# Optimization experiments

Hardware: AMD Instinct MI355X
Metric: run time of the kernel (lower is better)

The kernel has to match this reference:

```python
import jax, jax.numpy as jnp
import numpy as np


def setup_inputs() -> dict:
    key = jax.random.key(0)
    ks = jax.random.split(key, 4)
    N, T, D, H = 64, 512, 1024, 1024
    x = jax.random.normal(ks[0], (N, T, D), dtype=jnp.float32)
    h0 = jax.random.normal(ks[1], (N, H), dtype=jnp.float32)
    Wx = jax.random.normal(ks[2], (D, 4 * H), dtype=jnp.float32) / np.sqrt(D)
    Wh = jax.random.normal(ks[3], (H, 4 * H), dtype=jnp.float32) / np.sqrt(H)
    b = jnp.zeros((4 * H,), dtype=jnp.float32)
    return {"x": x, "h0": h0, "Wx": Wx, "Wh": Wh, "b": b}


def reference(x, h0, Wx, Wh, b):
    # x: [N, T, D]; h0: [N, H]; Wx: [D, 4H]; Wh: [H, 4H]; b: [4H]
    H = h0.shape[1]
    # Batch the input-to-hidden matmul over all timesteps at once: [N, T, 4H]
    xW = jnp.einsum('ntd,df->ntf', x, Wx) + b
    c0 = jnp.zeros_like(h0)

    def step(carry, xw_t):
        prev_h, prev_c = carry
        preact = xw_t + prev_h @ Wh           # [N, 4H]
        ai, af, ao, ag = jnp.split(preact, 4, axis=1)
        i = jax.nn.sigmoid(ai)
        f = jax.nn.sigmoid(af)
        o = jax.nn.sigmoid(ao)
        g = jnp.tanh(ag)
        next_c = f * prev_c + i * g
        next_h = o * jnp.tanh(next_c)
        return (next_h, next_c), next_h

    # scan over time: move T to leading axis
    _, hs = jax.lax.scan(step, (h0, c0), jnp.swapaxes(xW, 0, 1))
    return jnp.swapaxes(hs, 0, 1)  # [N, T, H]
```

## Files before the change

kernel.cpp:

```cpp
#include <hip/hip_runtime.h>
#include <cstdint>
#include <cstddef>

#define N_ 64
#define T_ 512
#define D_ 1024
#define H_ 1024
#define FH 4096

typedef __attribute__((ext_vector_type(8))) short bf16x8;
typedef __attribute__((ext_vector_type(4))) float f32x4;

static __device__ __forceinline__ uint16_t f2bf_(float f) {
  union { float f; uint32_t u; } v; v.f = f;
  uint32_t u = v.u + 0x7FFFu + ((v.u >> 16) & 1u);
  return (uint16_t)(u >> 16);
}
static __device__ __forceinline__ float bf2f_(uint16_t s) {
  union { uint32_t u; float f; } v; v.u = ((uint32_t)s) << 16;
  return v.f;
}
static __device__ __forceinline__ void unpk2_(unsigned long long e,
                                              uint32_t& hi, uint32_t& lo) {
  uint32_t a = (uint32_t)e, b = (uint32_t)(e >> 32);
  hi = (a >> 16) | (b & 0xFFFF0000u);
  lo = (a & 0xFFFFu) | (b << 16);
}
static __device__ __forceinline__ void cvt8_(const float* p, bf16x8& hv,
                                             bf16x8& lv) {
  float4 v0 = *reinterpret_cast<const float4*>(p);
  float4 v1 = *reinterpret_cast<const float4*>(p + 4);
  float f[8] = {v0.x, v0.y, v0.z, v0.w, v1.x, v1.y, v1.z, v1.w};
#pragma unroll
  for (int e = 0; e < 8; ++e) {
    ushort h = f2bf_(f[e]);
    hv[e] = (short)h;
    lv[e] = (short)f2bf_(f[e] - bf2f_(h));
  }
}

#define ALD(p) (*(p))

__global__ __launch_bounds__(256) void pack_w_k(const float* __restrict__ W,
                                                ushort* __restrict__ hi,
                                                ushort* __restrict__ lo) {
  const int i = blockIdx.x * 256 + threadIdx.x;
  const int lane = i & 63, kc = (i >> 6) & 31, bid = i >> 11;
  const int c = lane & 15;
  const int col = (c >> 2) * H_ + (bid << 2) + (c & 3);
  const int k0 = (kc << 5) + ((lane >> 4) << 3);
  const size_t o = ((size_t)(bid * 32 + kc) * 64 + lane) * 8;
#pragma unroll
  for (int e = 0; e < 8; ++e) {
    float v = W[(size_t)(k0 + e) * FH + col];
    ushort h = f2bf_(v);
    hi[o + e] = h;
    lo[o + e] = f2bf_(v - bf2f_(h));
  }
}

__global__ __launch_bounds__(256) void conv_h0pk_k(const float* __restrict__ src,
                                                   uint32_t* __restrict__ dst,
                                                   unsigned* bar) {
  if (blockIdx.x == 0) {
    bar[threadIdx.x] = 0u;
    if (threadIdx.x < 8) bar[384 + 32 * threadIdx.x] = 0u;
  }
  const int i = blockIdx.x * 256 + threadIdx.x;
  float4 v = reinterpret_cast<const float4*>(src)[i];
  uint4 o;
  { ushort h = f2bf_(v.x); o.x = ((uint32_t)h << 16) | f2bf_(v.x - bf2f_(h)); }
  { ushort h = f2bf_(v.y); o.y = ((uint32_t)h << 16) | f2bf_(v.y - bf2f_(h)); }
  { ushort h = f2bf_(v.z); o.z = ((uint32_t)h << 16) | f2bf_(v.z - bf2f_(h)); }
  { ushort h = f2bf_(v.w); o.w = ((uint32_t)h << 16) | f2bf_(v.w - bf2f_(h)); }
  reinterpret_cast<uint4*>(dst)[i] = o;
}

__global__ __launch_bounds__(256) void gemm_xw_mfma(
    const ushort* __restrict__ Wxh, const ushort* __restrict__ Wxl,
    const float* __restrict__ x, const float* __restrict__ bias,
    uint32_t* __restrict__ xwp, int tb) {
  const int bid = blockIdx.x;
  const int tl = blockIdx.y << 2;
  const int t0 = tb + tl;
  const int tid = threadIdx.x, lane = tid & 63, mt = tid >> 6;
  const int row = (mt << 4) | (lane & 15);
  const int kg = lane >> 4;

  const bf16x8* Bh = reinterpret_cast<const bf16x8*>(Wxh) + (size_t)bid * 2048 + lane;
  const bf16x8* Bl = reinterpret_cast<const bf16x8*>(Wxl) + (size_t)bid * 2048 + lane;
  const float* ax = x + ((size_t)row * T_ + t0) * D_ + (kg << 3);

  f32x4 xa0 = {0.f, 0.f, 0.f, 0.f};
  f32x4 xa1 = {0.f, 0.f, 0.f, 0.f};
  f32x4 xa2 = {0.f, 0.f, 0.f, 0.f};
  f32x4 xa3 = {0.f, 0.f, 0.f, 0.f};
#pragma unroll 2
  for (int kc = 0; kc < 32; ++kc) {
    bf16x8 bh = Bh[kc << 6];
    bf16x8 bl = Bl[kc << 6];
    bf16x8 h0, l0, h1, l1, h2, l2, h3, l3;
    cvt8_(ax + (kc << 5), h0, l0);
    cvt8_(ax + D_ + (kc << 5), h1, l1);
    cvt8_(ax + 2 * D_ + (kc << 5), h2, l2);
    cvt8_(ax + 3 * D_ + (kc << 5), h3, l3);
    xa0 = __builtin_amdgcn_mfma_f32_16x16x32_bf16(h0, bh, xa0, 0, 0, 0);
    xa1 = __builtin_amdgcn_mfma_f32_16x16x32_bf16(h1, bh, xa1, 0, 0, 0);
    xa2 = __builtin_amdgcn_mfma_f32_16x16x32_bf16(h2, bh, xa2, 0, 0, 0);
    xa3 = __builtin_amdgcn_mfma_f32_16x16x32_bf16(h3, bh, xa3, 0, 0, 0);
    xa0 = __builtin_amdgcn_mfma_f32_16x16x32_bf16(h0, bl, xa0, 0, 0, 0);
    xa1 = __builtin_amdgcn_mfma_f32_16x16x32_bf16(h1, bl, xa1, 0, 0, 0);
    xa2 = __builtin_amdgcn_mfma_f32_16x16x32_bf16(h2, bl, xa2, 0, 0, 0);
    xa3 = __builtin_amdgcn_mfma_f32_16x16x32_bf16(h3, bl, xa3, 0, 0, 0);
    xa0 = __builtin_amdgcn_mfma_f32_16x16x32_bf16(l0, bh, xa0, 0, 0, 0);
    xa1 = __builtin_amdgcn_mfma_f32_16x16x32_bf16(l1, bh, xa1, 0, 0, 0);
    xa2 = __builtin_amdgcn_mfma_f32_16x16x32_bf16(l2, bh, xa2, 0, 0, 0);
    xa3 = __builtin_amdgcn_mfma_f32_16x16x32_bf16(l3, bh, xa3, 0, 0, 0);
  }

  const int dc = lane & 15, dr = (lane >> 4) << 2;
  const int g = dc >> 2, jj = dc & 3;
  const float bv = bias[g * H_ + (bid << 2) + jj];
#pragma unroll
  for (int r = 0; r < 4; ++r) {
    const int rw = (mt << 4) + dr + r;
    const size_t o = ((size_t)tl * 256 + bid) * 1024 + rw * 16 + jj * 4 + g;
    float v0 = xa0[r] + bv, v1 = xa1[r] + bv, v2 = xa2[r] + bv, v3 = xa3[r] + bv;
    ushort h;
    h = f2bf_(v0); xwp[o] = ((uint32_t)h << 16) | f2bf_(v0 - bf2f_(h));
    h = f2bf_(v1); xwp[o + 262144] = ((uint32_t)h << 16) | f2bf_(v1 - bf2f_(h));
    h = f2bf_(v2); xwp[o + 2 * 262144] = ((uint32_t)h << 16) | f2bf_(v2 - bf2f_(h));
    h = f2bf_(v3); xwp[o + 3 * 262144] = ((uint32_t)h << 16) | f2bf_(v3 - bf2f_(h));
  }
}

__global__ __launch_bounds__(512, 2) void lstm_scan_k(
    const ushort* __restrict__ Whh_g, const ushort* __restrict__ Whl_g,
    const uint32_t* __restrict__ xwp,
    uint32_t* __restrict__ hseq, float* __restrict__ cbuf,
    float* __restrict__ out, unsigned* __restrict__ bar, int tb) {
  extern __shared__ char ldsraw[];
  bf16x8* const WhH = (bf16x8*)ldsraw;
  bf16x8* const WhL = WhH + 2048;
  float* const pre = (float*)(WhL + 2048);

  const int tid = threadIdx.x, bid = blockIdx.x;
  const int lane = tid & 63, w = tid >> 6;
  const int mt = w & 3, kh = w >> 2;
  const int khb = kh << 4;
  const int arow = (mt << 4) | (lane & 15);
  const int kg = lane >> 4;
  const int dc = lane & 15, dr = (lane >> 4) << 2;
  const int en = tid >> 2, ejj = tid & 3;

  unsigned* const relmy = bar + 384 + ((bid & 7) << 5);

  {
    const bf16x8* gh = reinterpret_cast<const bf16x8*>(Whh_g) + (size_t)bid * 2048;
    const bf16x8* gl = reinterpret_cast<const bf16x8*>(Whl_g) + (size_t)bid * 2048;
#pragma unroll
    for (int r = 0; r < 4; ++r) {
      int u = tid + (r << 9);
      WhH[u] = gh[u];
      WhL[u] = gl[u];
    }
  }
  __syncthreads();

  for (int tl = 0; tl < 256; ++tl) {
    const int t = tb + tl;
    f32x4 acc0 = {0.f, 0.f, 0.f, 0.f};
    f32x4 acc1 = {0.f, 0.f, 0.f, 0.f};
    const unsigned long long* Apk =
        (const unsigned long long*)(hseq + (size_t)t * 65536) +
        arow * 512 + (kh << 8) + kg * 4;

    unsigned long long pa0, pa1, pa2, pa3, pb0, pb1, pb2, pb3;
    unsigned long long pc0, pc1, pc2, pc3, pd0, pd1, pd2, pd3;
    unsigned long long qa0, qa1, qa2, qa3, qb0, qb1, qb2, qb3;
    unsigned long long qc0, qc1, qc2, qc3, qd0, qd1, qd2, qd3;

#define HLD(P, CH)                                                            \
  {                                                                           \
    const unsigned long long* ap_ = Apk + ((CH) << 6);                        \
    P##a0 = ALD(ap_ + 0);  P##a1 = ALD(ap_ + 1);                              \
    P##a2 = ALD(ap_ + 2);  P##a3 = ALD(ap_ + 3);                              \
    P##b0 = ALD(ap_ + 16); P##b1 = ALD(ap_ + 17);                             \
    P##b2 = ALD(ap_ + 18); P##b3 = ALD(ap_ + 19);                             \
    P##c0 = ALD(ap_ + 32); P##c1 = ALD(ap_ + 33);                             \
    P##c2 = ALD(ap_ + 34); P##c3 = ALD(ap_ + 35);                             \
    P##d0 = ALD(ap_ + 48); P##d1 = ALD(ap_ + 49);                             \
    P##d2 = ALD(ap_ + 50); P##d3 = ALD(ap_ + 51);                             \
  }

#define HKC(E0, E1, E2, E3, KCG, ACC)                                         \
  {                                                                           \
    union { uint32_t u[4]; bf16x8 v; } fh_, fl_;                              \
    unpk2_(E0, fh_.u[0], fl_.u[0]);                                           \
    unpk2_(E1, fh_.u[1], fl_.u[1]);                                           \
    unpk2_(E2, fh_.u[2], fl_.u[2]);                                           \
    unpk2_(E3, fh_.u[3], fl_.u[3]);                                           \
    bf16x8 bh_ = WhH[((KCG) << 6) + lane];                                    \
    bf16x8 bl_ = WhL[((KCG) << 6) + lane];                                    \
    ACC = __builtin_amdgcn_mfma_f32_16x16x32_bf16(fh_.v, bh_, ACC, 0, 0, 0);  \
    ACC = __builtin_amdgcn_mfma_f32_16x16x32_bf16(fh_.v, bl_, ACC, 0, 0, 0);  \
    ACC = __builtin_amdgcn_mfma_f32_16x16x32_bf16(fl_.v, bh_, ACC, 0, 0, 0);  \
  }

#define HCOMP(P, CH)                                                          \
  HKC(P##a0, P##a1, P##a2, P##a3, khb + (CH) * 4 + 0, acc0)                   \
  HKC(P##b0, P##b1, P##b2, P##b3, khb + (CH) * 4 + 1, acc1)                   \
  HKC(P##c0, P##c1, P##c2, P##c3, khb + (CH) * 4 + 2, acc0)                   \
  HKC(P##d0, P##d1, P##d2, P##d3, khb + (CH) * 4 + 3, acc1)

    HLD(p, 0)
    HLD(q, 1) HCOMP(p, 0)
    HLD(p, 2) HCOMP(q, 1)
    HLD(q, 3) HCOMP(p, 2)
    HCOMP(q, 3)
#undef HLD
#undef HKC
#undef HCOMP

    f32x4 accs = acc0 + acc1;
#pragma unroll
    for (int r = 0; r < 4; ++r)
      pre[((kh << 6) + (mt << 4) + dr + r) * 17 + dc] = accs[r];
    __syncthreads();

    if (tid < 256) {
      const uint4 xp = *reinterpret_cast<const uint4*>(
          xwp + (size_t)tl * 262144 + (size_t)bid * 1024 + en * 16 + ejj * 4);
      float a0 = pre[en * 17 + ejj] + pre[(64 + en) * 17 + ejj] +
                 bf2f_((ushort)(xp.x >> 16)) + bf2f_((ushort)(xp.x & 0xFFFF));
      float a1 = pre[en * 17 + 4 + ejj] + pre[(64 + en) * 17 + 4 + ejj] +
                 bf2f_((ushort)(xp.y >> 16)) + bf2f_((ushort)(xp.y & 0xFFFF));
      float a2 = pre[en * 17 + 8 + ejj] + pre[(64 + en) * 17 + 8 + ejj] +
                 bf2f_((ushort)(xp.z >> 16)) + bf2f_((ushort)(xp.z & 0xFFFF));
      float a3 = pre[en * 17 + 12 + ejj] + pre[(64 + en) * 17 + 12 + ejj] +
                 bf2f_((ushort)(xp.w >> 16)) + bf2f_((ushort)(xp.w & 0xFFFF));
      const int hx = en * H_ + (bid << 2) + ejj;
      float cp = (t == 0) ? 0.f : cbuf[hx];
      float iv = 1.f / (1.f + __expf(-a0));
      float fv = 1.f / (1.f + __expf(-a1));
      float ov = 1.f / (1.f + __expf(-a2));
      float gv = tanhf(a3);
      float cn = fmaf(fv, cp, iv * gv);
      cbuf[hx] = cn;
      float hn = ov * tanhf(cn);
      out[(size_t)en * ((size_t)T_ * H_) + (size_t)t * H_ + (bid << 2) + ejj] = hn;
      ushort hh = f2bf_(hn);
      uint32_t pk = ((uint32_t)hh << 16) | f2bf_(hn - bf2f_(hh));
      __hip_atomic_store(&hseq[(size_t)(t + 1) * 65536 + hx], pk,
                         __ATOMIC_RELAXED, __HIP_MEMORY_SCOPE_AGENT);
    }

    asm volatile("s_waitcnt vmcnt(0)" ::: "memory");
    __syncthreads();

    const unsigned tgt = (unsigned)(t + 1);
    if (tid == 0)
      __hip_atomic_store(&bar[bid], tgt, __ATOMIC_RELAXED,
                         __HIP_MEMORY_SCOPE_AGENT);
    if (bid == 0 && tid < 64) {
      const unsigned long long* fl = (const unsigned long long*)bar;
      for (;;) {
        unsigned long long v0 = __hip_atomic_load(fl + tid, __ATOMIC_RELAXED,
                                                  __HIP_MEMORY_SCOPE_AGENT);
        unsigned long long v1 = __hip_atomic_load(fl + 64 + tid, __ATOMIC_RELAXED,
                                                  __HIP_MEMORY_SCOPE_AGENT);
        bool ok = ((unsigned)v0 >= tgt) && ((unsigned)(v0 >> 32) >= tgt) &&
                  ((unsigned)v1 >= tgt) && ((unsigned)(v1 >> 32) >= tgt);
        if (__all((int)ok)) break;
      }
      if (tid < 8)
        __hip_atomic_store(bar + 384 + (tid << 5), tgt, __ATOMIC_RELAXED,
                           __HIP_MEMORY_SCOPE_AGENT);
    }
    if (tid == 0) {
      while (__hip_atomic_load(relmy, __ATOMIC_RELAXED,
                               __HIP_MEMORY_SCOPE_AGENT) < tgt)
        __builtin_amdgcn_s_sleep(1);
    }
    __syncthreads();
  }
}

__global__ __launch_bounds__(256) void lstm_step_fb(
    const float* __restrict__ xt, const float* __restrict__ Wx,
    const float* __restrict__ Wh, const float* __restrict__ bias,
    const float* __restrict__ h_prev, long long hstride,
    float* __restrict__ cbuf, float* __restrict__ h_out, int first) {
  __shared__ float hS[32][128];
  __shared__ float wT[32][132];
  __shared__ float pre[32][34];
  const int tid = threadIdx.x;
  const int colblk = blockIdx.x & 127;
  const int nh = blockIdx.x >> 7;
  const int j0 = colblk << 3;
  const int n0 = nh << 5;
  const int ng = tid >> 4, cg2 = tid & 15;
  const int na = ng << 1, ca = cg2 << 1;

  float acc[2][2] = {{0.f, 0.f}, {0.f, 0.f}};

#pragma unroll
  for (int pr = 0; pr < 2; ++pr) {
    const float* src = (pr == 0) ? h_prev : xt;
    long long sstr = (pr == 0) ? hstride : (long long)T_ * D_;
    const float* W = (pr == 0) ? Wh : Wx;
    for (int k0 = 0; k0 < 1024; k0 += 128) {
      __syncthreads();
#pragma unroll
      for (int p = 0; p < 4; ++p) {
        int idx = tid + (p << 8);
        int r = idx >> 5, c4 = (idx & 31) << 2;
        *reinterpret_cast<float4*>(&hS[r][c4]) =
            *reinterpret_cast<const float4*>(src + (size_t)(n0 + r) * sstr + k0 + c4);
      }
#pragma unroll
      for (int p = 0; p < 4; ++p) {
        int idx = tid + (p << 8);
        int k = idx >> 3, sub = idx & 7;
        int g = sub >> 1, hf = (sub & 1) << 2;
        float4 v = *reinterpret_cast<const float4*>(
            W + (size_t)(k0 + k) * FH + g * H_ + j0 + hf);
        int cb = (g << 3) + hf;
        wT[cb][k] = v.x; wT[cb + 1][k] = v.y; wT[cb + 2][k] = v.z; wT[cb + 3][k] = v.w;
      }
      __syncthreads();
#pragma unroll
      for (int kk = 0; kk < 128; kk += 4) {
        float4 h0v = *reinterpret_cast<const float4*>(&hS[na][kk]);
        float4 h1v = *reinterpret_cast<const float4*>(&hS[na + 1][kk]);
        float4 w0 = *reinterpret_cast<const float4*>(&wT[ca][kk]);
        float4 w1 = *reinterpret_cast<const float4*>(&wT[ca + 1][kk]);
        acc[0][0] = fmaf(h0v.x, w0.x, acc[0][0]); acc[0][0] = fmaf(h0v.y, w0.y, acc[0][0]);
        acc[0][0] = fmaf(h0v.z, w0.z, acc[0][0]); acc[0][0] = fmaf(h0v.w, w0.w, acc[0][0]);
        acc[0][1] = fmaf(h0v.x, w1.x, acc[0][1]); acc[0][1] = fmaf(h0v.y, w1.y, acc[0][1]);
        acc[0][1] = fmaf(h0v.z, w1.z, acc[0][1]); acc[0][1] = fmaf(h0v.w, w1.w, acc[0][1]);
        acc[1][0] = fmaf(h1v.x, w0.x, acc[1][0]); acc[1][0] = fmaf(h1v.y, w0.y, acc[1][0]);
        acc[1][0] = fmaf(h1v.z, w0.z, acc[1][0]); acc[1][0] = fmaf(h1v.w, w0.w, acc[1][0]);
        acc[1][1] = fmaf(h1v.x, w1.x, acc[1][1]); acc[1][1] = fmaf(h1v.y, w1.y, acc[1][1]);
        acc[1][1] = fmaf(h1v.z, w1.z, acc[1][1]); acc[1][1] = fmaf(h1v.w, w1.w, acc[1][1]);
      }
    }
  }

  pre[na][ca] = acc[0][0];
  pre[na][ca + 1] = acc[0][1];
  pre[na + 1][ca] = acc[1][0];
  pre[na + 1][ca + 1] = acc[1][1];
  __syncthreads();

  const int nl = tid >> 3, jl = tid & 7;
  const int n = n0 + nl;
  const int jg = j0 + jl;
  float ai = pre[nl][jl] + bias[jg];
  float af = pre[nl][8 + jl] + bias[H_ + jg];
  float ao = pre[nl][16 + jl] + bias[2 * H_ + jg];
  float ag = pre[nl][24 + jl] + bias[3 * H_ + jg];
  float cp = first ? 0.0f : cbuf[n * H_ + jg];
  float iv = 1.f / (1.f + __expf(-ai));
  float fv = 1.f / (1.f + __expf(-af));
  float ov = 1.f / (1.f + __expf(-ao));
  float gv = tanhf(ag);
  float cn = fmaf(fv, cp, iv * gv);
  cbuf[n * H_ + jg] = cn;
  h_out[(size_t)n * ((size_t)T_ * H_) + jg] = ov * tanhf(cn);
}

extern "C" void kernel_launch(void* const* d_in, const int* in_sizes, int n_in,
                              void* d_out, int out_size, void* d_ws, size_t ws_size,
                              hipStream_t stream) {
  (void)in_sizes; (void)n_in; (void)out_size;
  const float* x  = (const float*)d_in[0];
  const float* h0 = (const float*)d_in[1];
  const float* Wx = (const float*)d_in[2];
  const float* Wh = (const float*)d_in[3];
  const float* b  = (const float*)d_in[4];
  float* out = (float*)d_out;

  const size_t MB = 1u << 20;
  char* p = (char*)d_ws;

  if (ws_size >= 420 * MB) {
    unsigned* bar = (unsigned*)p;
    ushort* Whh = (ushort*)(p + 1 * MB);
    ushort* Whl = (ushort*)(p + 9 * MB);
    ushort* Wxh = (ushort*)(p + 17 * MB);
    ushort* Wxl = (ushort*)(p + 25 * MB);
    uint32_t* hseq = (uint32_t*)(p + 33 * MB);
    float* cbuf = (float*)(p + 162 * MB);
    uint32_t* xwp = (uint32_t*)(p + 163 * MB);

    pack_w_k<<<dim3(2048), dim3(256), 0, stream>>>(Wh, Whh, Whl);
    pack_w_k<<<dim3(2048), dim3(256), 0, stream>>>(Wx, Wxh, Wxl);
    conv_h0pk_k<<<dim3(64), dim3(256), 0, stream>>>(h0, hseq, bar);

    const unsigned SH = 2048 * 16 * 2 + 128 * 17 * 4;
    hipFuncSetAttribute((const void*)lstm_scan_k,
                        hipFuncAttributeMaxDynamicSharedMemorySize, (int)SH);

    gemm_xw_mfma<<<dim3(256, 64), dim3(256), 0, stream>>>(Wxh, Wxl, x, b, xwp, 0);
    lstm_scan_k<<<dim3(256), dim3(512), SH, stream>>>(Whh, Whl, xwp, hseq, cbuf,
                                                      out, bar, 0);
    gemm_xw_mfma<<<dim3(256, 64), dim3(256), 0, stream>>>(Wxh, Wxl, x, b, xwp, 256);
    lstm_scan_k<<<dim3(256), dim3(512), SH, stream>>>(Whh, Whl, xwp, hseq, cbuf,
                                                      out, bar, 256);
  } else {
    float* cbuf = (float*)p;
    for (int t = 0; t < T_; ++t) {
      const float* hp = (t == 0) ? h0 : out + (size_t)(t - 1) * H_;
      long long hstr = (t == 0) ? (long long)H_ : (long long)T_ * H_;
      lstm_step_fb<<<dim3(256), dim3(256), 0, stream>>>(
          x + (size_t)t * D_, Wx, Wh, b, hp, hstr, cbuf,
          out + (size_t)t * H_, t == 0);
    }
  }
}
```

Before: 9.381 ms.

## Pre-split x into bf16 hi/lo once and process time in four chunks

New measurement: 9.111 ms. 2.9% less time.

```diff
diff --git a/kernel.cpp b/kernel.cpp
--- a/kernel.cpp
+++ b/kernel.cpp
@@ -25,18 +25,6 @@
   uint32_t a = (uint32_t)e, b = (uint32_t)(e >> 32);
   hi = (a >> 16) | (b & 0xFFFF0000u);
   lo = (a & 0xFFFFu) | (b << 16);
-}
-static __device__ __forceinline__ void cvt8_(const float* p, bf16x8& hv,
-                                             bf16x8& lv) {
-  float4 v0 = *reinterpret_cast<const float4*>(p);
-  float4 v1 = *reinterpret_cast<const float4*>(p + 4);
-  float f[8] = {v0.x, v0.y, v0.z, v0.w, v1.x, v1.y, v1.z, v1.w};
-#pragma unroll
-  for (int e = 0; e < 8; ++e) {
-    ushort h = f2bf_(f[e]);
-    hv[e] = (short)h;
-    lv[e] = (short)f2bf_(f[e] - bf2f_(h));
-  }
 }
 
 #define ALD(p) (*(p))
@@ -59,6 +47,20 @@
   }
 }
 
+__global__ __launch_bounds__(256) void split_f32_k(const float* __restrict__ src,
+                                                   ushort* __restrict__ hi,
+                                                   ushort* __restrict__ lo) {
+  const size_t i = (size_t)blockIdx.x * 256 + threadIdx.x;
+  float4 v = reinterpret_cast<const float4*>(src)[i];
+  ushort4 h, l;
+  h.x = f2bf_(v.x); l.x = f2bf_(v.x - bf2f_(h.x));
+  h.y = f2bf_(v.y); l.y = f2bf_(v.y - bf2f_(h.y));
+  h.z = f2bf_(v.z); l.z = f2bf_(v.z - bf2f_(h.z));
+  h.w = f2bf_(v.w); l.w = f2bf_(v.w - bf2f_(h.w));
+  reinterpret_cast<ushort4*>(hi)[i] = h;
+  reinterpret_cast<ushort4*>(lo)[i] = l;
+}
+
 __global__ __launch_bounds__(256) void conv_h0pk_k(const float* __restrict__ src,
                                                    uint32_t* __restrict__ dst,
                                                    unsigned* bar) {
@@ -78,8 +80,8 @@
 
 __global__ __launch_bounds__(256) void gemm_xw_mfma(
     const ushort* __restrict__ Wxh, const ushort* __restrict__ Wxl,
-    const float* __restrict__ x, const float* __restrict__ bias,
-    uint32_t* __restrict__ xwp, int tb) {
+    const ushort* __restrict__ xh, const ushort* __restrict__ xl,
+    const float* __restrict__ bias, uint32_t* __restrict__ xwp, int tb) {
   const int bid = blockIdx.x;
   const int tl = blockIdx.y << 2;
   const int t0 = tb + tl;
@@ -89,7 +91,8 @@
 
   const bf16x8* Bh = reinterpret_cast<const bf16x8*>(Wxh) + (size_t)bid * 2048 + lane;
   const bf16x8* Bl = reinterpret_cast<const bf16x8*>(Wxl) + (size_t)bid * 2048 + lane;
-  const float* ax = x + ((size_t)row * T_ + t0) * D_ + (kg << 3);
+  const ushort* ah = xh + ((size_t)row * T_ + t0) * D_ + (kg << 3);
+  const ushort* al = xl + ((size_t)row * T_ + t0) * D_ + (kg << 3);
 
   f32x4 xa0 = {0.f, 0.f, 0.f, 0.f};
   f32x4 xa1 = {0.f, 0.f, 0.f, 0.f};
@@ -99,11 +102,14 @@
   for (int kc = 0; kc < 32; ++kc) {
     bf16x8 bh = Bh[kc << 6];
     bf16x8 bl = Bl[kc << 6];
-    bf16x8 h0, l0, h1, l1, h2, l2, h3, l3;
-    cvt8_(ax + (kc << 5), h0, l0);
-    cvt8_(ax + D_ + (kc << 5), h1, l1);
-    cvt8_(ax + 2 * D_ + (kc << 5), h2, l2);
-    cvt8_(ax + 3 * D_ + (kc << 5), h3, l3);
+    bf16x8 h0 = *reinterpret_cast<const bf16x8*>(ah + (kc << 5));
+    bf16x8 l0 = *reinterpret_cast<const bf16x8*>(al + (kc << 5));
+    bf16x8 h1 = *reinterpret_cast<const bf16x8*>(ah + D_ + (kc << 5));
+    bf16x8 l1 = *reinterpret_cast<const bf16x8*>(al + D_ + (kc << 5));
+    bf16x8 h2 = *reinterpret_cast<const bf16x8*>(ah + 2 * D_ + (kc << 5));
+    bf16x8 l2 = *reinterpret_cast<const bf16x8*>(al + 2 * D_ + (kc << 5));
+    bf16x8 h3 = *reinterpret_cast<const bf16x8*>(ah + 3 * D_ + (kc << 5));
+    bf16x8 l3 = *reinterpret_cast<const bf16x8*>(al + 3 * D_ + (kc << 5));
     xa0 = __builtin_amdgcn_mfma_f32_16x16x32_bf16(h0, bh, xa0, 0, 0, 0);
     xa1 = __builtin_amdgcn_mfma_f32_16x16x32_bf16(h1, bh, xa1, 0, 0, 0);
     xa2 = __builtin_amdgcn_mfma_f32_16x16x32_bf16(h2, bh, xa2, 0, 0, 0);
@@ -167,7 +173,7 @@
   }
   __syncthreads();
 
-  for (int tl = 0; tl < 256; ++tl) {
+  for (int tl = 0; tl < 128; ++tl) {
     const int t = tb + tl;
     f32x4 acc0 = {0.f, 0.f, 0.f, 0.f};
     f32x4 acc1 = {0.f, 0.f, 0.f, 0.f};
@@ -392,22 +398,26 @@
     ushort* Wxl = (ushort*)(p + 25 * MB);
     uint32_t* hseq = (uint32_t*)(p + 33 * MB);
     float* cbuf = (float*)(p + 162 * MB);
-    uint32_t* xwp = (uint32_t*)(p + 163 * MB);
+    ushort* xh = (ushort*)(p + 163 * MB);
+    ushort* xl = (ushort*)(p + 227 * MB);
+    uint32_t* xwp = (uint32_t*)(p + 291 * MB);
 
     pack_w_k<<<dim3(2048), dim3(256), 0, stream>>>(Wh, Whh, Whl);
     pack_w_k<<<dim3(2048), dim3(256), 0, stream>>>(Wx, Wxh, Wxl);
+    split_f32_k<<<dim3(32768), dim3(256), 0, stream>>>(x, xh, xl);
     conv_h0pk_k<<<dim3(64), dim3(256), 0, stream>>>(h0, hseq, bar);
 
     const unsigned SH = 2048 * 16 * 2 + 128 * 17 * 4;
     hipFuncSetAttribute((const void*)lstm_scan_k,
                         hipFuncAttributeMaxDynamicSharedMemorySize, (int)SH);
 
-    gemm_xw_mfma<<<dim3(256, 64), dim3(256), 0, stream>>>(Wxh, Wxl, x, b, xwp, 0);
-    lstm_scan_k<<<dim3(256), dim3(512), SH, stream>>>(Whh, Whl, xwp, hseq, cbuf,
-                                                      out, bar, 0);
-    gemm_xw_mfma<<<dim3(256, 64), dim3(256), 0, stream>>>(Wxh, Wxl, x, b, xwp, 256);
-    lstm_scan_k<<<dim3(256), dim3(512), SH, stream>>>(Whh, Whl, xwp, hseq, cbuf,
-                                                      out, bar, 256);
+    for (int c = 0; c < 4; ++c) {
+      const int tb = c * 128;
+      gemm_xw_mfma<<<dim3(256, 32), dim3(256), 0, stream>>>(Wxh, Wxl, xh, xl,
+                                                            b, xwp, tb);
+      lstm_scan_k<<<dim3(256), dim3(512), SH, stream>>>(Whh, Whl, xwp, hseq,
+                                                        cbuf, out, bar, tb);
+    }
   } else {
     float* cbuf = (float*)p;
     for (int t = 0; t < T_; ++t) {
```
